# Performance work log

Measured on AMD Instinct MI355X. Metric: run time of the kernel, lower is better.

## Reference

```python
import jax, jax.numpy as jnp
import numpy as np

SPLINE_ORDER = 3


def _bsplines(x, grid, k=SPLINE_ORDER):
    # x: [..., ]  grid: [G] (uniform, shared across in-features)
    # returns Cox-de Boor bases of order k: [..., G-1-k]
    x = x[..., None]
    bases = ((x >= grid[:-1]) & (x < grid[1:])).astype(x.dtype)
    for j in range(1, k + 1):
        left = (x - grid[: -(j + 1)]) / (grid[j:-1] - grid[: -(j + 1)]) * bases[..., :-1]
        right = (grid[j + 1:] - x) / (grid[j + 1:] - grid[1:-j]) * bases[..., 1:]
        bases = left + right
    return bases


def _kan_conv(x, base_w, spline_w, scaler, grid):
    # x: [B, C, H, W]; applies 5 independent KANLinear(9 -> 1) over 3x3 patches
    B, C, H, W = x.shape
    Ho, Wo = H - 2, W - 2
    patches = jax.lax.conv_general_dilated_patches(x, (3, 3), (1, 1), 'VALID')  # [B, C*9, Ho, Wo] (channel-major)
    p = patches.reshape(B, C, 9, Ho, Wo).transpose(0, 1, 3, 4, 2)  # [B, C, Ho, Wo, 9]
    sw = spline_w * scaler[..., None]  # [K, 9, S]
    sb = _bsplines(p, grid)            # [B, C, Ho, Wo, 9, S]
    out = (jnp.einsum('bchwi,ki->bchwk', jax.nn.silu(p), base_w)
           + jnp.einsum('bchwis,kis->bchwk', sb, sw))  # [B, C, Ho, Wo, K]
    # channel layout: for each input channel, the K conv outputs (c*K + k)
    return out.transpose(0, 1, 4, 2, 3).reshape(B, C * base_w.shape[0], Ho, Wo)


def _maxpool2(x):
    B, C, H, W = x.shape
    H2, W2 = H // 2, W // 2
    return x[:, :, :H2 * 2, :W2 * 2].reshape(B, C, H2, 2, W2, 2).max(axis=(3, 5))


def _forward(x, conv1_base, conv1_spline, conv1_scaler,
             conv2_base, conv2_spline, conv2_scaler,
             kan1_base, kan1_spline, kan1_scaler):
    dt = x.dtype
    # extended uniform grids (grid_range extended by spline_order*h on each side)
    grid1 = (jnp.arange(-3, 5 + 3 + 1, dtype=dt) * (2.0 / 5) - 1.0)    # grid_size=5,  range [-1,1], 12 pts
    grid2 = (jnp.arange(-3, 10 + 3 + 1, dtype=dt) * (2.0 / 10) - 1.0)  # grid_size=10, range [-1,1], 17 pts
    grid3 = (jnp.arange(-3, 10 + 3 + 1, dtype=dt) * (1.0 / 10))        # grid_size=10, range [0,1],  17 pts

    h = _kan_conv(x, conv1_base, conv1_spline, conv1_scaler, grid1)  # [B,5,26,26]
    h = _maxpool2(h)                                                  # [B,5,13,13]
    h = _kan_conv(h, conv2_base, conv2_spline, conv2_scaler, grid2)  # [B,25,11,11]
    h = _maxpool2(h)                                                  # [B,25,5,5]
    B = h.shape[0]
    f = h.reshape(B, -1)                                              # [B,625]

    sw = kan1_spline * kan1_scaler[..., None]                         # [10,625,13]
    sb = _bsplines(f, grid3)                                          # [B,625,13]
    logits = jax.nn.silu(f) @ kan1_base.T + jnp.einsum('bis,ois->bo', sb, sw)
    return jax.nn.log_softmax(logits, axis=1)


def setup_inputs() -> dict:
    key = jax.random.key(0)
    ks = jax.random.split(key, 10)
    d = jnp.float32
    return {
        'x': jax.random.uniform(ks[0], (1024, 1, 28, 28), dtype=d),
        'conv1_base': jax.random.normal(ks[1], (5, 9), dtype=d) * 0.3,
        'conv1_spline': jax.random.normal(ks[2], (5, 9, 8), dtype=d) * 0.1,
        'conv1_scaler': jax.random.normal(ks[3], (5, 9), dtype=d) * 0.3 + 1.0,
        'conv2_base': jax.random.normal(ks[4], (5, 9), dtype=d) * 0.3,
        'conv2_spline': jax.random.normal(ks[5], (5, 9, 13), dtype=d) * 0.1,
        'conv2_scaler': jax.random.normal(ks[6], (5, 9), dtype=d) * 0.3 + 1.0,
        'kan1_base': jax.random.normal(ks[7], (10, 625), dtype=d) * 0.05,
        'kan1_spline': jax.random.normal(ks[8], (10, 625, 13), dtype=d) * 0.05,
        'kan1_scaler': jax.random.normal(ks[9], (10, 625), dtype=d) * 0.3 + 1.0,
    }


def reference(x, conv1_base, conv1_spline, conv1_scaler,
              conv2_base, conv2_spline, conv2_scaler,
              kan1_base, kan1_spline, kan1_scaler):
    return _forward(x, conv1_base, conv1_spline, conv1_scaler,
                    conv2_base, conv2_spline, conv2_scaler,
                    kan1_base, kan1_spline, kan1_scaler)
```

## Files before the change

### kernel.cpp

```cpp
#include <hip/hip_runtime.h>

#define DEV __device__ __forceinline__

DEV float silu_f(float v) { return v / (1.0f + __expf(-v)); }

DEV int bspline4(float x, float g0, float inv_h, int imax, float w[4]) {
  float t = (x - g0) * inv_h;
  float fi = floorf(t);
  int i = (int)fi;
  if (t < 0.0f || i > imax) { w[0] = w[1] = w[2] = w[3] = 0.0f; return 0; }
  float u = t - fi;
  float u2 = u * u, u3 = u2 * u;
  float om = 1.0f - u;
  const float c6 = 1.0f / 6.0f;
  w[0] = om * om * om * c6;
  w[1] = (3.0f * u3 - 6.0f * u2 + 4.0f) * c6;
  w[2] = (-3.0f * u3 + 3.0f * u2 + 3.0f * u + 1.0f) * c6;
  w[3] = u3 * c6;
  return i - 3;
}

DEV float4 cubic_coeffs(float s0, float s1, float s2, float s3) {
  float4 c;
  const float c6 = 1.0f / 6.0f;
  c.x = (s0 + 4.0f * s1 + s2) * c6;
  c.y = (s2 - s0) * 0.5f;
  c.z = (s0 - 2.0f * s1 + s2) * 0.5f;
  c.w = (s3 - s0 + 3.0f * (s1 - s2)) * c6;
  return c;
}

DEV float enc_interval(float v, float g0, float inv_h, float tmax, float zslot) {
  const float t = (v - g0) * inv_h;
  return (t >= 0.0f && t < tmax) ? t : zslot;
}

__global__ __launch_bounds__(512, 8) void kkan_fused(
    const float* __restrict__ x,
    const float* __restrict__ c1b, const float* __restrict__ c1s, const float* __restrict__ c1sc,
    const float* __restrict__ c2b, const float* __restrict__ c2s, const float* __restrict__ c2sc,
    const float* __restrict__ kb,  const float* __restrict__ ks,  const float* __restrict__ ksc,
    float* __restrict__ out)
{
  __shared__ float4 tab1[540];
  __shared__ float4 tab2[765];
  __shared__ float2 pre1[784];
  __shared__ float2 pre2[845];
  __shared__ float  fv[625];
  __shared__ float  lred[8][10];
  __shared__ float  lfin[10];

  const int b = blockIdx.x;
  const int tid = threadIdx.x;

  const float4* xb4 = (const float4*)(x + b * 784);
  #pragma unroll 1
  for (int i = tid; i < 196; i += 512) {
    const float4 v4 = xb4[i];
    const float vs[4] = {v4.x, v4.y, v4.z, v4.w};
    #pragma unroll
    for (int j = 0; j < 4; ++j) {
      const float v = vs[j];
      pre1[i * 4 + j] = make_float2(silu_f(v),
                                    enc_interval(v, -2.2f, 2.5f, 11.0f, 11.5f));
    }
  }
  #pragma unroll 1
  for (int idx = tid; idx < 540; idx += 512) {
    const int tap = idx / 60, rem = idx % 60;
    const int k = rem / 12, iv = rem % 12;
    float4 c = make_float4(0.f, 0.f, 0.f, 0.f);
    if (iv <= 10) {
      const float sc = c1sc[k * 9 + tap];
      const float* sw = &c1s[(k * 9 + tap) * 8];
      float s[4];
      #pragma unroll
      for (int j = 0; j < 4; ++j) {
        const int m = iv - 3 + j;
        s[j] = ((unsigned)m < 8u) ? sw[m] * sc : 0.f;
      }
      c = cubic_coeffs(s[0], s[1], s[2], s[3]);
    }
    tab1[idx] = c;
  }
  #pragma unroll 1
  for (int idx = tid; idx < 765; idx += 512) {
    const int tap = idx / 85, rem = idx % 85;
    const int k = rem / 17, iv = rem % 17;
    float4 c = make_float4(0.f, 0.f, 0.f, 0.f);
    if (iv <= 15) {
      const float sc = c2sc[k * 9 + tap];
      const float* sw = &c2s[(k * 9 + tap) * 13];
      float s[4];
      #pragma unroll
      for (int j = 0; j < 4; ++j) {
        const int m = iv - 3 + j;
        s[j] = ((unsigned)m < 13u) ? sw[m] * sc : 0.f;
      }
      c = cubic_coeffs(s[0], s[1], s[2], s[3]);
    }
    tab2[idx] = c;
  }
  __syncthreads();

  #pragma unroll 1
  for (int q = tid; q < 676; q += 512) {
    const int pos = q >> 2, quad = q & 3;
    const int pi = pos / 13, pj = pos % 13;
    const int oh = 2 * pi + (quad >> 1), ow = 2 * pj + (quad & 1);
    float acc[5] = {0.f, 0.f, 0.f, 0.f, 0.f};
    #pragma unroll 1
    for (int kh = 0; kh < 3; ++kh) {
      #pragma unroll 1
      for (int kw = 0; kw < 3; ++kw) {
        const int tap = kh * 3 + kw;
        const float2 pc = pre1[(oh + kh) * 28 + (ow + kw)];
        const float sil = pc.x;
        const float fi = floorf(pc.y);
        const int ic = (int)fi;
        const float u = pc.y - fi;
        const float4* tp = &tab1[tap * 60 + ic];
        const float* bw = &c1b[tap];
        #pragma unroll
        for (int k = 0; k < 5; ++k) {
          const float4 c = tp[k * 12];
          const float sp = ((c.w * u + c.z) * u + c.y) * u + c.x;
          acc[k] += sil * bw[k * 9] + sp;
        }
      }
    }
    #pragma unroll
    for (int k = 0; k < 5; ++k) {
      float m = acc[k];
      m = fmaxf(m, __shfl_xor(m, 1));
      m = fmaxf(m, __shfl_xor(m, 2));
      if (quad == 0) {
        pre2[(k * 13 + pi) * 13 + pj] =
            make_float2(silu_f(m), enc_interval(m, -1.6f, 5.0f, 16.0f, 16.5f));
      }
    }
  }
  __syncthreads();

  if (tid < 500) {
    const int pos = tid >> 2, quad = tid & 3;
    const int c = pos / 25, rr = pos % 25;
    const int y = rr / 5, xx = rr % 5;
    const int oh = 2 * y + (quad >> 1), ow = 2 * xx + (quad & 1);
    float acc[5] = {0.f, 0.f, 0.f, 0.f, 0.f};
    #pragma unroll 1
    for (int kh = 0; kh < 3; ++kh) {
      #pragma unroll 1
      for (int kw = 0; kw < 3; ++kw) {
        const int tap = kh * 3 + kw;
        const float2 pc = pre2[(c * 13 + oh + kh) * 13 + (ow + kw)];
        const float sil = pc.x;
        const float fi = floorf(pc.y);
        const int ic = (int)fi;
        const float u = pc.y - fi;
        const float4* tp = &tab2[tap * 85 + ic];
        const float* bw = &c2b[tap];
        #pragma unroll
        for (int k = 0; k < 5; ++k) {
          const float4 cc = tp[k * 17];
          const float sp = ((cc.w * u + cc.z) * u + cc.y) * u + cc.x;
          acc[k] += sil * bw[k * 9] + sp;
        }
      }
    }
    #pragma unroll
    for (int k = 0; k < 5; ++k) {
      float m = acc[k];
      m = fmaxf(m, __shfl_xor(m, 1));
      m = fmaxf(m, __shfl_xor(m, 2));
      if (quad == 0) fv[(c * 5 + k) * 25 + rr] = m;
    }
  }
  __syncthreads();

  float acc[10] = {0.f, 0.f, 0.f, 0.f, 0.f, 0.f, 0.f, 0.f, 0.f, 0.f};
  #pragma unroll 1
  for (int i = tid; i < 625; i += 512) {
    const float v = fv[i];
    const float sil = silu_f(v);
    float w[4];
    const int m0 = bspline4(v, -0.3f, 10.0f, 15, w);
    int idx[4];
    #pragma unroll
    for (int j = 0; j < 4; ++j) {
      const int m = m0 + j;
      const bool ok = ((unsigned)m < 13u);
      idx[j] = ok ? m : 0;
      w[j] = ok ? w[j] : 0.f;
    }
    #pragma unroll 2
    for (int o = 0; o < 10; ++o) {
      const int wi = o * 625 + i;
      const float* sp = ks + (size_t)wi * 13;
      const float s = w[0] * sp[idx[0]] + w[1] * sp[idx[1]]
                    + w[2] * sp[idx[2]] + w[3] * sp[idx[3]];
      acc[o] += sil * kb[wi] + s * ksc[wi];
    }
  }
  #pragma unroll
  for (int o = 0; o < 10; ++o) {
    float v = acc[o];
    for (int off = 32; off > 0; off >>= 1) v += __shfl_down(v, off);
    acc[o] = v;
  }
  const int wave = tid >> 6, lane = tid & 63;
  if (lane == 0) {
    #pragma unroll
    for (int o = 0; o < 10; ++o) lred[wave][o] = acc[o];
  }
  __syncthreads();
  if (tid < 10) {
    float s = 0.f;
    #pragma unroll
    for (int wv = 0; wv < 8; ++wv) s += lred[wv][tid];
    lfin[tid] = s;
  }
  __syncthreads();
  if (tid == 0) {
    float mx = lfin[0];
    #pragma unroll
    for (int o = 1; o < 10; ++o) mx = fmaxf(mx, lfin[o]);
    float s = 0.f;
    #pragma unroll
    for (int o = 0; o < 10; ++o) s += __expf(lfin[o] - mx);
    const float ls = logf(s) + mx;
    #pragma unroll
    for (int o = 0; o < 10; ++o) out[b * 10 + o] = lfin[o] - ls;
  }
}

extern "C" void kernel_launch(void* const* d_in, const int* in_sizes, int n_in,
                              void* d_out, int out_size, void* d_ws, size_t ws_size,
                              hipStream_t stream) {
  (void)n_in; (void)d_ws; (void)ws_size; (void)out_size;
  const float* x    = (const float*)d_in[0];
  const float* c1b  = (const float*)d_in[1];
  const float* c1s  = (const float*)d_in[2];
  const float* c1sc = (const float*)d_in[3];
  const float* c2b  = (const float*)d_in[4];
  const float* c2s  = (const float*)d_in[5];
  const float* c2sc = (const float*)d_in[6];
  const float* kb   = (const float*)d_in[7];
  const float* ks   = (const float*)d_in[8];
  const float* ksc  = (const float*)d_in[9];
  float* out = (float*)d_out;

  const int B = in_sizes[0] / 784;
  kkan_fused<<<dim3(B), dim3(512), 0, stream>>>(
      x, c1b, c1s, c1sc, c2b, c2s, c2sc, kb, ks, ksc, out);
}
```

Before: 39.64 us.

## Stage final KAN spline weights through shared memory per output row

The final KANLinear stage used to gather spline weights straight from global memory, with adjacent threads reading 13-float-strided rows. It now loops over the 10 outputs and has the whole block copy each 8125-float weight slab into shared memory with coalesced loads, then gathers from LDS. Each thread's B-spline weights and indices for its up to two inputs are computed once, before the loop. To fit the slab, shared memory becomes one aliased buffer whose earlier tables are reused. This adds 20 block barriers and moves every weight in each slab rather than only the needed taps.

```diff
diff --git a/kernel.cpp b/kernel.cpp
--- a/kernel.cpp
+++ b/kernel.cpp
@@ -42,13 +42,16 @@
     const float* __restrict__ kb,  const float* __restrict__ ks,  const float* __restrict__ ksc,
     float* __restrict__ out)
 {
-  __shared__ float4 tab1[540];
-  __shared__ float4 tab2[765];
-  __shared__ float2 pre1[784];
-  __shared__ float2 pre2[845];
-  __shared__ float  fv[625];
-  __shared__ float  lred[8][10];
-  __shared__ float  lfin[10];
+  __shared__ __align__(16) char smem[36864];
+  float* fv   = (float*)smem;
+  float* lred = fv + 625;
+  float* lfin = lred + 80;
+  char* ph = smem + 2880;
+  float4* tab1 = (float4*)ph;
+  float4* tab2 = tab1 + 540;
+  float2* pre1 = (float2*)(ph + 20880);
+  float2* pre2 = (float2*)(ph + 27152);
+  float* sw = (float*)ph;
 
   const int b = blockIdx.x;
   const int tid = threadIdx.x;
@@ -72,12 +75,12 @@
     float4 c = make_float4(0.f, 0.f, 0.f, 0.f);
     if (iv <= 10) {
       const float sc = c1sc[k * 9 + tap];
-      const float* sw = &c1s[(k * 9 + tap) * 8];
+      const float* swp = &c1s[(k * 9 + tap) * 8];
       float s[4];
       #pragma unroll
       for (int j = 0; j < 4; ++j) {
         const int m = iv - 3 + j;
-        s[j] = ((unsigned)m < 8u) ? sw[m] * sc : 0.f;
+        s[j] = ((unsigned)m < 8u) ? swp[m] * sc : 0.f;
       }
       c = cubic_coeffs(s[0], s[1], s[2], s[3]);
     }
@@ -90,12 +93,12 @@
     float4 c = make_float4(0.f, 0.f, 0.f, 0.f);
     if (iv <= 15) {
       const float sc = c2sc[k * 9 + tap];
-      const float* sw = &c2s[(k * 9 + tap) * 13];
+      const float* swp = &c2s[(k * 9 + tap) * 13];
       float s[4];
       #pragma unroll
       for (int j = 0; j < 4; ++j) {
         const int m = iv - 3 + j;
-        s[j] = ((unsigned)m < 13u) ? sw[m] * sc : 0.f;
+        s[j] = ((unsigned)m < 13u) ? swp[m] * sc : 0.f;
       }
       c = cubic_coeffs(s[0], s[1], s[2], s[3]);
     }
@@ -178,30 +181,58 @@
   }
   __syncthreads();
 
-  float acc[10] = {0.f, 0.f, 0.f, 0.f, 0.f, 0.f, 0.f, 0.f, 0.f, 0.f};
-  #pragma unroll 1
-  for (int i = tid; i < 625; i += 512) {
-    const float v = fv[i];
-    const float sil = silu_f(v);
-    float w[4];
-    const int m0 = bspline4(v, -0.3f, 10.0f, 15, w);
-    int idx[4];
+  const int i1 = tid, i2 = tid + 512;
+  const bool has1 = (i1 < 625), has2 = (i2 < 625);
+  float sil1 = 0.f, sil2 = 0.f;
+  float w1[4] = {0.f, 0.f, 0.f, 0.f}, w2[4] = {0.f, 0.f, 0.f, 0.f};
+  int id1[4] = {0, 0, 0, 0}, id2[4] = {0, 0, 0, 0};
+  if (has1) {
+    const float v = fv[i1];
+    sil1 = silu_f(v);
+    const int m0 = bspline4(v, -0.3f, 10.0f, 15, w1);
     #pragma unroll
     for (int j = 0; j < 4; ++j) {
       const int m = m0 + j;
       const bool ok = ((unsigned)m < 13u);
-      idx[j] = ok ? m : 0;
-      w[j] = ok ? w[j] : 0.f;
-    }
-    #pragma unroll 2
-    for (int o = 0; o < 10; ++o) {
-      const int wi = o * 625 + i;
-      const float* sp = ks + (size_t)wi * 13;
-      const float s = w[0] * sp[idx[0]] + w[1] * sp[idx[1]]
-                    + w[2] * sp[idx[2]] + w[3] * sp[idx[3]];
-      acc[o] += sil * kb[wi] + s * ksc[wi];
-    }
-  }
+      id1[j] = i1 * 13 + (ok ? m : 0);
+      w1[j] = ok ? w1[j] : 0.f;
+    }
+  }
+  if (has2) {
+    const float v = fv[i2];
+    sil2 = silu_f(v);
+    const int m0 = bspline4(v, -0.3f, 10.0f, 15, w2);
+    #pragma unroll
+    for (int j = 0; j < 4; ++j) {
+      const int m = m0 + j;
+      const bool ok = ((unsigned)m < 13u);
+      id2[j] = i2 * 13 + (ok ? m : 0);
+      w2[j] = ok ? w2[j] : 0.f;
+    }
+  }
+
+  float acc[10];
+  #pragma unroll 1
+  for (int o = 0; o < 10; ++o) {
+    __syncthreads();
+    const float* ko = ks + o * 8125;
+    #pragma unroll 1
+    for (int j = tid; j < 8125; j += 512) sw[j] = ko[j];
+    __syncthreads();
+    float a = 0.f;
+    if (has1) {
+      const float s = w1[0] * sw[id1[0]] + w1[1] * sw[id1[1]]
+                    + w1[2] * sw[id1[2]] + w1[3] * sw[id1[3]];
+      a = sil1 * kb[o * 625 + i1] + s * ksc[o * 625 + i1];
+    }
+    if (has2) {
+      const float s = w2[0] * sw[id2[0]] + w2[1] * sw[id2[1]]
+                    + w2[2] * sw[id2[2]] + w2[3] * sw[id2[3]];
+      a += sil2 * kb[o * 625 + i2] + s * ksc[o * 625 + i2];
+    }
+    acc[o] = a;
+  }
+
   #pragma unroll
   for (int o = 0; o < 10; ++o) {
     float v = acc[o];
@@ -211,13 +242,13 @@
   const int wave = tid >> 6, lane = tid & 63;
   if (lane == 0) {
     #pragma unroll
-    for (int o = 0; o < 10; ++o) lred[wave][o] = acc[o];
+    for (int o = 0; o < 10; ++o) lred[wave * 10 + o] = acc[o];
   }
   __syncthreads();
   if (tid < 10) {
     float s = 0.f;
     #pragma unroll
-    for (int wv = 0; wv < 8; ++wv) s += lred[wv][tid];
+    for (int wv = 0; wv < 8; ++wv) s += lred[wv * 10 + tid];
     lfin[tid] = s;
   }
   __syncthreads();
```

Result: slower. 48.22 us (+21.6%).
